# Optimization experiments

Hardware: AMD Instinct MI355X
Metric: run time of the kernel (lower is better)

## Reference

```python
import jax, jax.numpy as jnp
import numpy as np

N_HASHES = 4
CHUNK = 144
REDUCTION = 4
RES_SCALE = 1.0
NORM_EPS = 5e-5


def conv2d(x, w, b, pad):
    y = jax.lax.conv_general_dilated(
        x, w, window_strides=(1, 1), padding=[(pad, pad), (pad, pad)],
        dimension_numbers=('NCHW', 'OIHW', 'NCHW'))
    return y + b[None, :, None, None]


def add_adjacent_buckets(x):
    # x: (N, h, n_chunks, chunk, e); concat each chunk with its circular neighbors
    back = jnp.roll(x, 1, axis=2)
    fwd = jnp.roll(x, -1, axis=2)
    return jnp.concatenate([x, back, fwd], axis=3)


def setup_inputs() -> dict:
    key = jax.random.key(0)
    ks = jax.random.split(key, 6)
    x = jax.random.normal(ks[0], (1, 32, 192, 192), jnp.float32)
    w_match = jax.random.normal(ks[1], (8, 32, 3, 3), jnp.float32) * 0.05
    b_match = jnp.zeros((8,), jnp.float32)
    w_asm = jax.random.normal(ks[2], (32, 32, 1, 1), jnp.float32) * 0.05
    b_asm = jnp.zeros((32,), jnp.float32)
    rotations = jax.random.normal(ks[3], (8, N_HASHES, 64), jnp.float32)
    return {'x': x, 'w_match': w_match, 'b_match': b_match,
            'w_asm': w_asm, 'b_asm': b_asm, 'rotations': rotations}


def reference(x, w_match, b_match, w_asm, b_asm, rotations):
    N, _, H, W = x.shape
    L = H * W
    # conv_match: 3x3 conv 32->8; conv_assembly: 1x1 conv 32->32
    x_embed = conv2d(x, w_match, b_match, 1).reshape(N, -1, L).transpose(0, 2, 1)  # (N, L, 8)
    y_embed = conv2d(x, w_asm, b_asm, 0).reshape(N, -1, L).transpose(0, 2, 1)      # (N, L, 32)
    C = x_embed.shape[-1]
    hash_buckets = min(L // CHUNK + (L // CHUNK) % 2, 128)  # = 128 here

    # --- LSH hashing (non-differentiable; rotations passed in for determinism) ---
    rotated = jnp.einsum('blf,fhi->bhli', x_embed, rotations)        # (N, h, L, hb/2)
    rotated = jnp.concatenate([rotated, -rotated], axis=-1)          # (N, h, L, hb)
    hash_codes = jnp.argmax(rotated, axis=-1)                        # (N, h, L)
    hash_codes = hash_codes + (jnp.arange(N_HASHES) * hash_buckets)[None, :, None]
    hash_codes = hash_codes.reshape(N, -1)                           # (N, h*L)

    # --- sort tokens by bucket id ---
    indices = jnp.argsort(hash_codes, axis=-1)
    undo_sort = jnp.argsort(indices, axis=-1)
    mod_indices = indices % L
    x_sorted = jnp.take_along_axis(x_embed, mod_indices[:, :, None], axis=1)  # (N, h*L, 8)
    y_sorted = jnp.take_along_axis(y_embed, mod_indices[:, :, None], axis=1)  # (N, h*L, 32)

    x_b = x_sorted.reshape(N, N_HASHES, -1, C)
    y_b = y_sorted.reshape(N, N_HASHES, -1, C * REDUCTION)
    padding = (-L) % CHUNK  # static; 0 for L=192*192
    if padding:
        x_b = jnp.concatenate([x_b, x_b[:, :, -padding:, :]], axis=2)
        y_b = jnp.concatenate([y_b, y_b[:, :, -padding:, :]], axis=2)
    x_b = x_b.reshape(N, N_HASHES, -1, CHUNK, C)
    y_b = y_b.reshape(N, N_HASHES, -1, CHUNK, C * REDUCTION)

    # --- bucketed attention with adjacent buckets ---
    nrm = jnp.linalg.norm(x_b, axis=-1, keepdims=True)
    x_match = x_b / jnp.maximum(nrm, NORM_EPS)   # F.normalize(eps=5e-5)
    x_match = add_adjacent_buckets(x_match)      # (N, h, k, 3*chunk, 8)
    y_adj = add_adjacent_buckets(y_b)            # (N, h, k, 3*chunk, 32)

    raw = jnp.einsum('bhkie,bhkje->bhkij', x_b, x_match)  # (N, h, k, 144, 432)
    bucket_score = jax.scipy.special.logsumexp(raw, axis=-1, keepdims=True)
    score = jnp.exp(raw - bucket_score)
    ret = jnp.einsum('bhkij,bhkje->bhkie', score, y_adj)  # (N, h, k, 144, 32)

    ret = ret.reshape(N, N_HASHES, -1, C * REDUCTION)
    bucket_score = bucket_score.reshape(N, N_HASHES, -1)
    if padding:
        ret = ret[:, :, :-padding, :]
        bucket_score = bucket_score[:, :, :-padding]
    ret = ret.reshape(N, -1, C * REDUCTION)
    bucket_score = bucket_score.reshape(N, -1)

    # --- unsort and combine hash rounds via softmax over logsumexp scores ---
    ret = jnp.take_along_axis(ret, undo_sort[:, :, None], axis=1)
    bucket_score = jnp.take_along_axis(bucket_score, undo_sort, axis=1)
    ret = ret.reshape(N, N_HASHES, L, C * REDUCTION)
    probs = jax.nn.softmax(bucket_score.reshape(N, N_HASHES, L, 1), axis=1)
    out = jnp.sum(ret * probs, axis=1)                     # (N, L, 32)
    out = out.transpose(0, 2, 1).reshape(N, -1, H, W) * RES_SCALE + x
    return out
```

## Files before the change

### kernel.cpp

```cpp
#include <hip/hip_runtime.h>
#include <hip/hip_bf16.h>
#include <math.h>

#define LTOT 36864
#define NH 4
#define NCHUNK 256
#define CHU 144
#define NBUCK 128
#define NSEG 144
#define HW_ 192
#define VTS 148

typedef unsigned int u32;
typedef unsigned short u16;
typedef unsigned long long u64;
typedef __attribute__((ext_vector_type(4))) short short4v;
typedef __attribute__((ext_vector_type(4))) float f32x4;

__device__ __forceinline__ u32 pkbf(float a, float b){
  union { __hip_bfloat162 h2; u32 u; } cv;
  cv.h2 = __float22bfloat162_rn(float2{a,b});
  return cv.u;
}
__device__ __forceinline__ float bflo(u32 w){ return __uint_as_float(w<<16); }
__device__ __forceinline__ float bfhi(u32 w){ return __uint_as_float(w & 0xffff0000u); }

__global__ __launch_bounds__(256) void k_conv(const float* __restrict__ x,
    const float* __restrict__ wm, const float* __restrict__ bm,
    const float* __restrict__ wa, const float* __restrict__ ba,
    float* __restrict__ xe, float* __restrict__ ye)
{
  __shared__ float xs[32*108];
  const int t = threadIdx.x;
  const int id = blockIdx.x;

  if (id < 576){
    const int bx = id % 12, by = id / 12;
    for (int idx=t; idx<3456; idx+=256){
      int ci = idx/108, rem = idx-ci*108;
      int iy = rem/18,  ix = rem-iy*18;
      int yy = by*4+iy-1, xx = bx*16+ix-1;
      float v = 0.f;
      if (yy>=0 && yy<HW_ && xx>=0 && xx<HW_) v = x[ci*LTOT + yy*HW_ + xx];
      xs[idx] = v;
    }
    __syncthreads();
    const int lane = t & 63;
    const int co0 = __builtin_amdgcn_readfirstlane((t>>6)<<1);
    const int ix = lane & 15, iy = lane >> 4;
    float a0 = bm[co0], a1 = bm[co0+1];
    const float* xb  = xs + iy*18 + ix;
    const float* w0p = wm + co0*288;
    const float* w1p = w0p + 288;
    for (int ci=0; ci<32; ci++){
      const float* xp = xb + ci*108;
      float x00=xp[0],  x01=xp[1],  x02=xp[2];
      float x10=xp[18], x11=xp[19], x12=xp[20];
      float x20=xp[36], x21=xp[37], x22=xp[38];
      const float* w0 = w0p + ci*9;
      const float* w1 = w1p + ci*9;
      a0 += x00*w0[0]+x01*w0[1]+x02*w0[2]
          + x10*w0[3]+x11*w0[4]+x12*w0[5]
          + x20*w0[6]+x21*w0[7]+x22*w0[8];
      a1 += x00*w1[0]+x01*w1[1]+x02*w1[2]
          + x10*w1[3]+x11*w1[4]+x12*w1[5]
          + x20*w1[6]+x21*w1[7]+x22*w1[8];
    }
    const int l = (by*4+iy)*HW_ + bx*16+ix;
    *(float2*)(xe + l*8 + co0) = float2{a0,a1};
  } else {
    const int zid = id - 576;
    const int cb = (zid/144)*8;
    const int l  = (zid%144)*256 + t;
    float acc[8];
    #pragma unroll
    for (int co=0;co<8;co++) acc[co] = ba[cb+co];
    #pragma unroll 4
    for (int ci=0; ci<32; ci++){
      float xv = x[ci*LTOT + l];
      #pragma unroll
      for (int co=0;co<8;co++) acc[co] += xv * wa[(cb+co)*32 + ci];
    }
    float4* yp = (float4*)(ye + l*32 + cb);
    yp[0] = make_float4(acc[0],acc[1],acc[2],acc[3]);
    yp[1] = make_float4(acc[4],acc[5],acc[6],acc[7]);
  }
}

__global__ __launch_bounds__(256) void k_hashrank(const float* __restrict__ xe,
    const float* __restrict__ rot, int* __restrict__ code,
    int* __restrict__ lrank, int* __restrict__ hist)
{
  const int h = blockIdx.y, seg = blockIdx.x, t = threadIdx.x;
  const int l = seg*256 + t;
  const float4* qp = (const float4*)(xe + l*8);
  float4 qa = qp[0], qb = qp[1];
  float best = -INFINITY; int bi = 0;
  float worst = INFINITY; int wi = 0;
  for (int i=0; i<64; i++){
    const float* rp = rot + h*64 + i;
    float v = qa.x*rp[0]    + qa.y*rp[256]  + qa.z*rp[512]  + qa.w*rp[768]
            + qb.x*rp[1024] + qb.y*rp[1280] + qb.z*rp[1536] + qb.w*rp[1792];
    if (v > best)  { best  = v; bi = i; }
    if (v < worst) { worst = v; wi = i; }
  }
  int c = (-worst > best) ? (64+wi) : bi;
  code[h*LTOT + l] = c;

  const int lane = t & 63, w = t >> 6;
  u64 mask = ~0ull;
  #pragma unroll
  for (int bit=0; bit<7; bit++){
    u64 bset = __ballot((c>>bit)&1);
    mask &= ((c>>bit)&1) ? bset : ~bset;
  }
  int rin = __popcll(mask & ((lane==0)?0ull:(~0ull >> (64-lane))));
  int cnt = __popcll(mask);

  __shared__ int wh[4][NBUCK];
  ((int*)wh)[t] = 0; ((int*)wh)[t+256] = 0;
  __syncthreads();
  if (rin == 0) wh[w][c] = cnt;
  __syncthreads();
  int r = rin;
  for (int ww=0; ww<w; ww++) r += wh[ww][c];
  lrank[h*LTOT + l] = r;
  if (t < NBUCK) hist[(h*NSEG+seg)*NBUCK + t] = wh[0][t]+wh[1][t]+wh[2][t]+wh[3][t];
}

__global__ __launch_bounds__(512) void k_scan(const int* __restrict__ hist,
    int* __restrict__ segoff)
{
  const int h = blockIdx.x;
  const int b = threadIdx.x & 127, g = threadIdx.x >> 7;
  int vals[36];
  int sum = 0;
  #pragma unroll
  for (int i=0;i<36;i++){
    vals[i] = hist[(h*NSEG + g*36 + i)*NBUCK + b];
    sum += vals[i];
  }
  __shared__ int ps[4][NBUCK];
  __shared__ int tot[NBUCK];
  __shared__ int scv[NBUCK];
  ps[g][b] = sum;
  __syncthreads();
  if (g == 0){
    int run = 0;
    #pragma unroll
    for (int gg=0; gg<4; gg++){ int tv = ps[gg][b]; ps[gg][b] = run; run += tv; }
    tot[b] = run;
    int v = run;
    #pragma unroll
    for (int off=1; off<64; off<<=1){
      int u = __shfl_up(v, off);
      if ((b & 63) >= off) v += u;
    }
    scv[b] = v;
  }
  __syncthreads();
  int base = scv[b] - tot[b] + ((b >= 64) ? scv[63] : 0);
  int run2 = base + ps[g][b];
  #pragma unroll
  for (int i=0;i<36;i++){
    segoff[(h*NSEG + g*36 + i)*NBUCK + b] = run2;
    run2 += vals[i];
  }
}

__global__ __launch_bounds__(256) void k_scatter(const int* __restrict__ code,
    const int* __restrict__ lrank, const int* __restrict__ segoff,
    const float* __restrict__ xe, const float* __restrict__ ye,
    int* __restrict__ rankof, u16* __restrict__ Ks, u16* __restrict__ Qs,
    u16* __restrict__ Vs)
{
  const int h = blockIdx.y, seg = blockIdx.x, t = threadIdx.x;
  const int l = seg*256 + t;
  int c = code[h*LTOT + l];
  int r = segoff[(h*NSEG+seg)*NBUCK + c] + lrank[h*LTOT + l];
  rankof[h*LTOT + l] = r;

  const float4* xr = (const float4*)(xe + l*8);
  float4 a = xr[0], b = xr[1];
  float n2 = a.x*a.x+a.y*a.y+a.z*a.z+a.w*a.w
           + b.x*b.x+b.y*b.y+b.z*b.z+b.w*b.w;
  float sc = 1.0f / fmaxf(sqrtf(n2), 5e-5f);
  uint4 kk, qq;
  kk.x = pkbf(a.x*sc,a.y*sc); kk.y = pkbf(a.z*sc,a.w*sc);
  kk.z = pkbf(b.x*sc,b.y*sc); kk.w = pkbf(b.z*sc,b.w*sc);
  qq.x = pkbf(a.x,a.y); qq.y = pkbf(a.z,a.w);
  qq.z = pkbf(b.x,b.y); qq.w = pkbf(b.z,b.w);
  *(uint4*)(Ks + (size_t)(h*LTOT + r)*8) = kk;
  *(uint4*)(Qs + (size_t)(h*LTOT + r)*8) = qq;

  const float4* yr = (const float4*)(ye + l*32);
  uint4* vp = (uint4*)(Vs + (size_t)(h*LTOT + r)*32);
  #pragma unroll
  for (int e4=0; e4<4; e4++){
    float4 v0 = yr[2*e4], v1 = yr[2*e4+1];
    uint4 w;
    w.x = pkbf(v0.x,v0.y); w.y = pkbf(v0.z,v0.w);
    w.z = pkbf(v1.x,v1.y); w.w = pkbf(v1.z,v1.w);
    vp[e4] = w;
  }
}

__global__ __launch_bounds__(320) void k_attn(const u16* __restrict__ Ks,
    const u16* __restrict__ Qs, const u16* __restrict__ Vs,
    u16* __restrict__ ret_s, float* __restrict__ bs_s)
{
  __shared__ __align__(16) u16 Klds[CHU*8];
  __shared__ __align__(16) u16 Qlds[CHU*8];
  __shared__ __align__(16) u16 VT[32*VTS];
  __shared__ float qn[CHU];

  const int t = threadIdx.x;
  const int k = blockIdx.x, h = blockIdx.y;

  if (t < CHU){
    uint4 qv = *(const uint4*)(Qs + (size_t)(h*LTOT + k*CHU + t)*8);
    *(uint4*)(Qlds + t*8) = qv;
    float f0=bflo(qv.x), f1=bfhi(qv.x), f2=bflo(qv.y), f3=bfhi(qv.y);
    float f4=bflo(qv.z), f5=bfhi(qv.z), f6=bflo(qv.w), f7=bfhi(qv.w);
    float n2 = f0*f0+f1*f1+f2*f2+f3*f3+f4*f4+f5*f5+f6*f6+f7*f7;
    qn[t] = sqrtf(n2)*1.01f + 1e-6f;
  }
  __syncthreads();

  const int lane = t & 63;
  const int wv = t >> 6;
  const int q = lane & 15;
  const int quad = lane >> 4;
  const int tl0 = 2*wv, tl1 = (2*wv+1 < 9) ? 2*wv+1 : 8;

  const short4v zs = {0,0,0,0};
  short4v bq0 = zs, bq1 = zs;
  if (quad < 2){
    bq0 = *(const short4v*)(Qlds + (tl0*16+q)*8 + quad*4);
    bq1 = *(const short4v*)(Qlds + (tl1*16+q)*8 + quad*4);
  }
  const float m0 = qn[tl0*16+q], m1 = qn[tl1*16+q];

  f32x4 o00={0,0,0,0}, o01={0,0,0,0}, o10={0,0,0,0}, o11={0,0,0,0};
  float s0 = 0.f, s1 = 0.f;

  for (int r=0; r<3; r++){
    __syncthreads();
    const int gkb = ((k + NCHUNK-1 + r) & (NCHUNK-1)) * CHU;
    if (t < CHU){
      *(uint4*)(Klds + t*8) = *(const uint4*)(Ks + (size_t)(h*LTOT + gkb + t)*8);
    } else if (t >= 176){
      int i = t - 176;
      int p = i >> 1, hf = i & 1;
      const uint4* ra = (const uint4*)(Vs + (size_t)(h*LTOT + gkb + 2*p)*32);
      const uint4* rb = (const uint4*)(Vs + (size_t)(h*LTOT + gkb + 2*p+1)*32);
      uint4 A0 = ra[hf*2], A1 = ra[hf*2+1];
      uint4 B0 = rb[hf*2], B1 = rb[hf*2+1];
      u32 aw[8] = {A0.x,A0.y,A0.z,A0.w,A1.x,A1.y,A1.z,A1.w};
      u32 bw[8] = {B0.x,B0.y,B0.z,B0.w,B1.x,B1.y,B1.z,B1.w};
      int ebase = hf*16;
      #pragma unroll
      for (int m=0;m<8;m++){
        u32 al = aw[m]&0xffffu, ah = aw[m]>>16;
        u32 bl = bw[m]&0xffffu, bh = bw[m]>>16;
        *(u32*)&VT[(ebase+2*m  )*VTS + 2*p] = al | (bl<<16);
        *(u32*)&VT[(ebase+2*m+1)*VTS + 2*p] = ah | (bh<<16);
      }
    }
    __syncthreads();

    #pragma unroll 3
    for (int kt=0; kt<9; kt++){
      short4v av = zs;
      if (quad < 2) av = *(const short4v*)(Klds + (kt*16+q)*8 + quad*4);
      f32x4 zc = {0.f,0.f,0.f,0.f};
      f32x4 stA = __builtin_amdgcn_mfma_f32_16x16x16bf16_1k(av, bq0, zc, 0,0,0);
      f32x4 stB = __builtin_amdgcn_mfma_f32_16x16x16bf16_1k(av, bq1, zc, 0,0,0);

      float pA0 = __expf(stA[0]-m0), pA1 = __expf(stA[1]-m0);
      float pA2 = __expf(stA[2]-m0), pA3 = __expf(stA[3]-m0);
      float pB0 = __expf(stB[0]-m1), pB1 = __expf(stB[1]-m1);
      float pB2 = __expf(stB[2]-m1), pB3 = __expf(stB[3]-m1);
      s0 += (pA0+pA1)+(pA2+pA3);
      s1 += (pB0+pB1)+(pB2+pB3);

      union { u32 u[2]; short4v s4; } pkA, pkB;
      pkA.u[0] = pkbf(pA0,pA1); pkA.u[1] = pkbf(pA2,pA3);
      pkB.u[0] = pkbf(pB0,pB1); pkB.u[1] = pkbf(pB2,pB3);

      short4v va0 = *(const short4v*)(&VT[ q    *VTS + kt*16 + quad*4]);
      short4v va1 = *(const short4v*)(&VT[(q+16)*VTS + kt*16 + quad*4]);
      o00 = __builtin_amdgcn_mfma_f32_16x16x16bf16_1k(va0, pkA.s4, o00, 0,0,0);
      o01 = __builtin_amdgcn_mfma_f32_16x16x16bf16_1k(va1, pkA.s4, o01, 0,0,0);
      o10 = __builtin_amdgcn_mfma_f32_16x16x16bf16_1k(va0, pkB.s4, o10, 0,0,0);
      o11 = __builtin_amdgcn_mfma_f32_16x16x16bf16_1k(va1, pkB.s4, o11, 0,0,0);
    }
  }

  float st0 = s0, st1 = s1;
  st0 += __shfl_xor(st0, 16); st0 += __shfl_xor(st0, 32);
  st1 += __shfl_xor(st1, 16); st1 += __shfl_xor(st1, 32);
  float inv0 = 1.0f/st0, inv1 = 1.0f/st1;

  const int row0 = h*LTOT + k*CHU + tl0*16 + q;
  const int row1 = h*LTOT + k*CHU + tl1*16 + q;
  u16* rp0 = ret_s + (size_t)row0*32;
  u16* rp1 = ret_s + (size_t)row1*32;
  uint2 wA, wB;
  wA.x = pkbf(o00[0]*inv0, o00[1]*inv0); wA.y = pkbf(o00[2]*inv0, o00[3]*inv0);
  wB.x = pkbf(o01[0]*inv0, o01[1]*inv0); wB.y = pkbf(o01[2]*inv0, o01[3]*inv0);
  *(uint2*)&rp0[quad*4]    = wA;
  *(uint2*)&rp0[16+quad*4] = wB;
  wA.x = pkbf(o10[0]*inv1, o10[1]*inv1); wA.y = pkbf(o10[2]*inv1, o10[3]*inv1);
  wB.x = pkbf(o11[0]*inv1, o11[1]*inv1); wB.y = pkbf(o11[2]*inv1, o11[3]*inv1);
  *(uint2*)&rp1[quad*4]    = wA;
  *(uint2*)&rp1[16+quad*4] = wB;
  if (quad == 0){
    bs_s[row0] = m0 + __logf(st0);
    bs_s[row1] = m1 + __logf(st1);
  }
}

__global__ __launch_bounds__(256) void k_final(const float* __restrict__ x,
    const int* __restrict__ rankof, const u16* __restrict__ ret_s,
    const float* __restrict__ bs_s, float* __restrict__ out)
{
  const int l  = blockIdx.x*64 + (threadIdx.x & 63);
  const int eg = threadIdx.x >> 6;
  int r[NH]; float bs[NH];
  #pragma unroll
  for (int h=0;h<NH;h++) r[h] = rankof[h*LTOT + l];
  #pragma unroll
  for (int h=0;h<NH;h++) bs[h] = bs_s[h*LTOT + r[h]];
  float m = fmaxf(fmaxf(bs[0],bs[1]), fmaxf(bs[2],bs[3]));
  float p[NH]; float s = 0.f;
  #pragma unroll
  for (int h=0;h<NH;h++){ p[h] = __expf(bs[h]-m); s += p[h]; }
  float inv = 1.0f/s;
  float o[8];
  #pragma unroll
  for (int e=0;e<8;e++) o[e]=0.f;
  #pragma unroll
  for (int h=0;h<NH;h++){
    float w = p[h]*inv;
    uint4 v = *(const uint4*)(ret_s + (size_t)(h*LTOT + r[h])*32 + eg*8);
    o[0] += w*bflo(v.x); o[1] += w*bfhi(v.x);
    o[2] += w*bflo(v.y); o[3] += w*bfhi(v.y);
    o[4] += w*bflo(v.z); o[5] += w*bfhi(v.z);
    o[6] += w*bflo(v.w); o[7] += w*bfhi(v.w);
  }
  #pragma unroll
  for (int e=0;e<8;e++){
    int ge = eg*8 + e;
    out[ge*LTOT + l] = o[e] + x[ge*LTOT + l];
  }
}

extern "C" void kernel_launch(void* const* d_in, const int* in_sizes, int n_in,
                              void* d_out, int out_size, void* d_ws, size_t ws_size,
                              hipStream_t stream)
{
  const float* x   = (const float*)d_in[0];
  const float* wm  = (const float*)d_in[1];
  const float* bm  = (const float*)d_in[2];
  const float* wa  = (const float*)d_in[3];
  const float* ba  = (const float*)d_in[4];
  const float* rot = (const float*)d_in[5];
  float* out = (float*)d_out;

  char* ws = (char*)d_ws;
  size_t off = 0;
  auto alloc = [&](size_t bytes)->void*{
    void* p = ws + off;
    off = (off + bytes + 255) & ~(size_t)255;
    return p;
  };
  float* xe     = (float*)alloc((size_t)LTOT*8*4);
  float* ye     = (float*)alloc((size_t)LTOT*32*4);
  int*   code   = (int*)  alloc((size_t)NH*LTOT*4);
  int*   lrank  = (int*)  alloc((size_t)NH*LTOT*4);
  int*   hist   = (int*)  alloc((size_t)NH*NSEG*NBUCK*4);
  int*   segoff = (int*)  alloc((size_t)NH*NSEG*NBUCK*4);
  int*   rankof = (int*)  alloc((size_t)NH*LTOT*4);
  u16*   Ks     = (u16*)  alloc((size_t)NH*LTOT*8*2);
  u16*   Qs     = (u16*)  alloc((size_t)NH*LTOT*8*2);
  u16*   Vs     = (u16*)  alloc((size_t)NH*LTOT*32*2);
  u16*   ret_s  = (u16*)  alloc((size_t)NH*LTOT*32*2);
  float* bs_s   = (float*)alloc((size_t)NH*LTOT*4);

  hipLaunchKernelGGL(k_conv,     dim3(1152),       dim3(256), 0, stream, x, wm, bm, wa, ba, xe, ye);
  hipLaunchKernelGGL(k_hashrank, dim3(NSEG,NH),    dim3(256), 0, stream, xe, rot, code, lrank, hist);
  hipLaunchKernelGGL(k_scan,     dim3(NH),         dim3(512), 0, stream, hist, segoff);
  hipLaunchKernelGGL(k_scatter,  dim3(NSEG,NH),    dim3(256), 0, stream, code, lrank, segoff, xe, ye, rankof, Ks, Qs, Vs);
  hipLaunchKernelGGL(k_attn,     dim3(NCHUNK,NH),  dim3(320), 0, stream, Ks, Qs, Vs, ret_s, bs_s);
  hipLaunchKernelGGL(k_final,    dim3(576),        dim3(256), 0, stream, x, rankof, ret_s, bs_s, out);
}
```

Measured before the change: 137.5 us.

## Fuse 1x1 conv into 3x3 conv tiles and prefetch next K/V chunk in attention

The 1x1 assembly conv is merged into the 3x3 conv blocks, reusing the center pixel already staged in shared memory, so the separate blocks that reread x from global memory are gone and the grid is halved. In the attention kernel, the K/V chunk for the next neighbor round is loaded into registers before the MFMA loop over the current chunk and written to LDS afterwards. This hides global load latency behind compute. The costs are extra registers for the prefetched data and fewer conv blocks, each doing more work.

```diff
diff --git a/kernel.cpp b/kernel.cpp
--- a/kernel.cpp
+++ b/kernel.cpp
@@ -33,58 +33,51 @@
   __shared__ float xs[32*108];
   const int t = threadIdx.x;
   const int id = blockIdx.x;
-
-  if (id < 576){
-    const int bx = id % 12, by = id / 12;
-    for (int idx=t; idx<3456; idx+=256){
-      int ci = idx/108, rem = idx-ci*108;
-      int iy = rem/18,  ix = rem-iy*18;
-      int yy = by*4+iy-1, xx = bx*16+ix-1;
-      float v = 0.f;
-      if (yy>=0 && yy<HW_ && xx>=0 && xx<HW_) v = x[ci*LTOT + yy*HW_ + xx];
-      xs[idx] = v;
-    }
-    __syncthreads();
-    const int lane = t & 63;
-    const int co0 = __builtin_amdgcn_readfirstlane((t>>6)<<1);
-    const int ix = lane & 15, iy = lane >> 4;
-    float a0 = bm[co0], a1 = bm[co0+1];
-    const float* xb  = xs + iy*18 + ix;
-    const float* w0p = wm + co0*288;
-    const float* w1p = w0p + 288;
-    for (int ci=0; ci<32; ci++){
-      const float* xp = xb + ci*108;
-      float x00=xp[0],  x01=xp[1],  x02=xp[2];
-      float x10=xp[18], x11=xp[19], x12=xp[20];
-      float x20=xp[36], x21=xp[37], x22=xp[38];
-      const float* w0 = w0p + ci*9;
-      const float* w1 = w1p + ci*9;
-      a0 += x00*w0[0]+x01*w0[1]+x02*w0[2]
-          + x10*w0[3]+x11*w0[4]+x12*w0[5]
-          + x20*w0[6]+x21*w0[7]+x22*w0[8];
-      a1 += x00*w1[0]+x01*w1[1]+x02*w1[2]
-          + x10*w1[3]+x11*w1[4]+x12*w1[5]
-          + x20*w1[6]+x21*w1[7]+x22*w1[8];
-    }
-    const int l = (by*4+iy)*HW_ + bx*16+ix;
-    *(float2*)(xe + l*8 + co0) = float2{a0,a1};
-  } else {
-    const int zid = id - 576;
-    const int cb = (zid/144)*8;
-    const int l  = (zid%144)*256 + t;
-    float acc[8];
+  const int bx = id % 12, by = id / 12;
+
+  for (int idx=t; idx<3456; idx+=256){
+    int ci = idx/108, rem = idx-ci*108;
+    int iy = rem/18,  ix = rem-iy*18;
+    int yy = by*4+iy-1, xx = bx*16+ix-1;
+    float v = 0.f;
+    if (yy>=0 && yy<HW_ && xx>=0 && xx<HW_) v = x[ci*LTOT + yy*HW_ + xx];
+    xs[idx] = v;
+  }
+  __syncthreads();
+  const int lane = t & 63;
+  const int w  = __builtin_amdgcn_readfirstlane(t>>6);
+  const int co0 = 2*w;
+  const int cb  = 8*w;
+  const int ix = lane & 15, iy = lane >> 4;
+  float a0 = bm[co0], a1 = bm[co0+1];
+  float acc[8];
+  #pragma unroll
+  for (int co=0;co<8;co++) acc[co] = ba[cb+co];
+  const float* xb  = xs + iy*18 + ix;
+  const float* w0p = wm + co0*288;
+  const float* w1p = w0p + 288;
+  for (int ci=0; ci<32; ci++){
+    const float* xp = xb + ci*108;
+    float x00=xp[0],  x01=xp[1],  x02=xp[2];
+    float x10=xp[18], x11=xp[19], x12=xp[20];
+    float x20=xp[36], x21=xp[37], x22=xp[38];
+    const float* w0 = w0p + ci*9;
+    const float* w1 = w1p + ci*9;
+    a0 += x00*w0[0]+x01*w0[1]+x02*w0[2]
+        + x10*w0[3]+x11*w0[4]+x12*w0[5]
+        + x20*w0[6]+x21*w0[7]+x22*w0[8];
+    a1 += x00*w1[0]+x01*w1[1]+x02*w1[2]
+        + x10*w1[3]+x11*w1[4]+x12*w1[5]
+        + x20*w1[6]+x21*w1[7]+x22*w1[8];
+    const float* wap = wa + cb*32 + ci;
     #pragma unroll
-    for (int co=0;co<8;co++) acc[co] = ba[cb+co];
-    #pragma unroll 4
-    for (int ci=0; ci<32; ci++){
-      float xv = x[ci*LTOT + l];
-      #pragma unroll
-      for (int co=0;co<8;co++) acc[co] += xv * wa[(cb+co)*32 + ci];
-    }
-    float4* yp = (float4*)(ye + l*32 + cb);
-    yp[0] = make_float4(acc[0],acc[1],acc[2],acc[3]);
-    yp[1] = make_float4(acc[4],acc[5],acc[6],acc[7]);
-  }
+    for (int co=0;co<8;co++) acc[co] += x11 * wap[co*32];
+  }
+  const int l = (by*4+iy)*HW_ + bx*16+ix;
+  *(float2*)(xe + l*8 + co0) = float2{a0,a1};
+  float4* yp = (float4*)(ye + l*32 + cb);
+  yp[0] = make_float4(acc[0],acc[1],acc[2],acc[3]);
+  yp[1] = make_float4(acc[4],acc[5],acc[6],acc[7]);
 }
 
 __global__ __launch_bounds__(256) void k_hashrank(const float* __restrict__ xe,
@@ -217,13 +210,39 @@
   const int t = threadIdx.x;
   const int k = blockIdx.x, h = blockIdx.y;
 
+  uint4 kpref;
+  uint4 vpa0, vpa1, vpb0, vpb1;
+  const int vp_i = t - 176, vp_p = vp_i >> 1, vp_hf = vp_i & 1;
+
+  {
+    const int gkb = ((k + NCHUNK-1) & (NCHUNK-1)) * CHU;
+    if (t < CHU){
+      kpref = *(const uint4*)(Ks + (size_t)(h*LTOT + gkb + t)*8);
+      uint4 qv = *(const uint4*)(Qs + (size_t)(h*LTOT + k*CHU + t)*8);
+      *(uint4*)(Qlds + t*8) = qv;
+      float f0=bflo(qv.x), f1=bfhi(qv.x), f2=bflo(qv.y), f3=bfhi(qv.y);
+      float f4=bflo(qv.z), f5=bfhi(qv.z), f6=bflo(qv.w), f7=bfhi(qv.w);
+      qn[t] = sqrtf(f0*f0+f1*f1+f2*f2+f3*f3+f4*f4+f5*f5+f6*f6+f7*f7)*1.01f + 1e-6f;
+    } else if (t >= 176){
+      const uint4* ra = (const uint4*)(Vs + (size_t)(h*LTOT + gkb + 2*vp_p)*32);
+      const uint4* rb = (const uint4*)(Vs + (size_t)(h*LTOT + gkb + 2*vp_p+1)*32);
+      vpa0 = ra[vp_hf*2]; vpa1 = ra[vp_hf*2+1];
+      vpb0 = rb[vp_hf*2]; vpb1 = rb[vp_hf*2+1];
+    }
+  }
   if (t < CHU){
-    uint4 qv = *(const uint4*)(Qs + (size_t)(h*LTOT + k*CHU + t)*8);
-    *(uint4*)(Qlds + t*8) = qv;
-    float f0=bflo(qv.x), f1=bfhi(qv.x), f2=bflo(qv.y), f3=bfhi(qv.y);
-    float f4=bflo(qv.z), f5=bfhi(qv.z), f6=bflo(qv.w), f7=bfhi(qv.w);
-    float n2 = f0*f0+f1*f1+f2*f2+f3*f3+f4*f4+f5*f5+f6*f6+f7*f7;
-    qn[t] = sqrtf(n2)*1.01f + 1e-6f;
+    *(uint4*)(Klds + t*8) = kpref;
+  } else if (t >= 176){
+    u32 aw[8] = {vpa0.x,vpa0.y,vpa0.z,vpa0.w,vpa1.x,vpa1.y,vpa1.z,vpa1.w};
+    u32 bw[8] = {vpb0.x,vpb0.y,vpb0.z,vpb0.w,vpb1.x,vpb1.y,vpb1.z,vpb1.w};
+    int ebase = vp_hf*16;
+    #pragma unroll
+    for (int m=0;m<8;m++){
+      u32 al = aw[m]&0xffffu, ah = aw[m]>>16;
+      u32 bl = bw[m]&0xffffu, bh = bw[m]>>16;
+      *(u32*)&VT[(ebase+2*m  )*VTS + 2*vp_p] = al | (bl<<16);
+      *(u32*)&VT[(ebase+2*m+1)*VTS + 2*vp_p] = ah | (bh<<16);
+    }
   }
   __syncthreads();
 
@@ -245,29 +264,17 @@
   float s0 = 0.f, s1 = 0.f;
 
   for (int r=0; r<3; r++){
-    __syncthreads();
-    const int gkb = ((k + NCHUNK-1 + r) & (NCHUNK-1)) * CHU;
-    if (t < CHU){
-      *(uint4*)(Klds + t*8) = *(const uint4*)(Ks + (size_t)(h*LTOT + gkb + t)*8);
-    } else if (t >= 176){
-      int i = t - 176;
-      int p = i >> 1, hf = i & 1;
-      const uint4* ra = (const uint4*)(Vs + (size_t)(h*LTOT + gkb + 2*p)*32);
-      const uint4* rb = (const uint4*)(Vs + (size_t)(h*LTOT + gkb + 2*p+1)*32);
-      uint4 A0 = ra[hf*2], A1 = ra[hf*2+1];
-      uint4 B0 = rb[hf*2], B1 = rb[hf*2+1];
-      u32 aw[8] = {A0.x,A0.y,A0.z,A0.w,A1.x,A1.y,A1.z,A1.w};
-      u32 bw[8] = {B0.x,B0.y,B0.z,B0.w,B1.x,B1.y,B1.z,B1.w};
-      int ebase = hf*16;
-      #pragma unroll
-      for (int m=0;m<8;m++){
-        u32 al = aw[m]&0xffffu, ah = aw[m]>>16;
-        u32 bl = bw[m]&0xffffu, bh = bw[m]>>16;
-        *(u32*)&VT[(ebase+2*m  )*VTS + 2*p] = al | (bl<<16);
-        *(u32*)&VT[(ebase+2*m+1)*VTS + 2*p] = ah | (bh<<16);
+    if (r < 2){
+      const int gkb = ((k + NCHUNK + r) & (NCHUNK-1)) * CHU;
+      if (t < CHU){
+        kpref = *(const uint4*)(Ks + (size_t)(h*LTOT + gkb + t)*8);
+      } else if (t >= 176){
+        const uint4* ra = (const uint4*)(Vs + (size_t)(h*LTOT + gkb + 2*vp_p)*32);
+        const uint4* rb = (const uint4*)(Vs + (size_t)(h*LTOT + gkb + 2*vp_p+1)*32);
+        vpa0 = ra[vp_hf*2]; vpa1 = ra[vp_hf*2+1];
+        vpb0 = rb[vp_hf*2]; vpb1 = rb[vp_hf*2+1];
       }
     }
-    __syncthreads();
 
     #pragma unroll 3
     for (int kt=0; kt<9; kt++){
@@ -294,6 +301,25 @@
       o01 = __builtin_amdgcn_mfma_f32_16x16x16bf16_1k(va1, pkA.s4, o01, 0,0,0);
       o10 = __builtin_amdgcn_mfma_f32_16x16x16bf16_1k(va0, pkB.s4, o10, 0,0,0);
       o11 = __builtin_amdgcn_mfma_f32_16x16x16bf16_1k(va1, pkB.s4, o11, 0,0,0);
+    }
+
+    if (r < 2){
+      __syncthreads();
+      if (t < CHU){
+        *(uint4*)(Klds + t*8) = kpref;
+      } else if (t >= 176){
+        u32 aw[8] = {vpa0.x,vpa0.y,vpa0.z,vpa0.w,vpa1.x,vpa1.y,vpa1.z,vpa1.w};
+        u32 bw[8] = {vpb0.x,vpb0.y,vpb0.z,vpb0.w,vpb1.x,vpb1.y,vpb1.z,vpb1.w};
+        int ebase = vp_hf*16;
+        #pragma unroll
+        for (int m=0;m<8;m++){
+          u32 al = aw[m]&0xffffu, ah = aw[m]>>16;
+          u32 bl = bw[m]&0xffffu, bh = bw[m]>>16;
+          *(u32*)&VT[(ebase+2*m  )*VTS + 2*vp_p] = al | (bl<<16);
+          *(u32*)&VT[(ebase+2*m+1)*VTS + 2*vp_p] = ah | (bh<<16);
+        }
+      }
+      __syncthreads();
     }
   }
 
@@ -388,7 +414,7 @@
   u16*   ret_s  = (u16*)  alloc((size_t)NH*LTOT*32*2);
   float* bs_s   = (float*)alloc((size_t)NH*LTOT*4);
 
-  hipLaunchKernelGGL(k_conv,     dim3(1152),       dim3(256), 0, stream, x, wm, bm, wa, ba, xe, ye);
+  hipLaunchKernelGGL(k_conv,     dim3(576),        dim3(256), 0, stream, x, wm, bm, wa, ba, xe, ye);
   hipLaunchKernelGGL(k_hashrank, dim3(NSEG,NH),    dim3(256), 0, stream, xe, rot, code, lrank, hist);
   hipLaunchKernelGGL(k_scan,     dim3(NH),         dim3(512), 0, stream, hist, segoff);
   hipLaunchKernelGGL(k_scatter,  dim3(NSEG,NH),    dim3(256), 0, stream, code, lrank, segoff, xe, ye, rankof, Ks, Qs, Vs);
```

After: 140.2 us. Within noise of the previous version (+1.9%).

## Fuse 1x1 conv into 3x3 conv, scatter attention outputs to unsorted positions

Applied to the files above, without the earlier changes.

The 1x1 assembly conv is now computed inside the 3x3 conv blocks, reusing the shared-memory center pixel and writing bf16 values directly. The scatter kernel then copies them instead of converting. The attention kernel writes its outputs and logsumexp scores straight to original token positions through an inverse permutation, so the final kernel reads contiguously with no rank gather. The last wave also skips the duplicated ninth tile. The trade-offs are scattered writes in attention and heavier per-thread work in the conv kernel.

```diff
diff --git a/kernel.cpp b/kernel.cpp
--- a/kernel.cpp
+++ b/kernel.cpp
@@ -28,63 +28,56 @@
 __global__ __launch_bounds__(256) void k_conv(const float* __restrict__ x,
     const float* __restrict__ wm, const float* __restrict__ bm,
     const float* __restrict__ wa, const float* __restrict__ ba,
-    float* __restrict__ xe, float* __restrict__ ye)
+    float* __restrict__ xe, u16* __restrict__ Vu)
 {
   __shared__ float xs[32*108];
   const int t = threadIdx.x;
   const int id = blockIdx.x;
-
-  if (id < 576){
-    const int bx = id % 12, by = id / 12;
-    for (int idx=t; idx<3456; idx+=256){
-      int ci = idx/108, rem = idx-ci*108;
-      int iy = rem/18,  ix = rem-iy*18;
-      int yy = by*4+iy-1, xx = bx*16+ix-1;
-      float v = 0.f;
-      if (yy>=0 && yy<HW_ && xx>=0 && xx<HW_) v = x[ci*LTOT + yy*HW_ + xx];
-      xs[idx] = v;
-    }
-    __syncthreads();
-    const int lane = t & 63;
-    const int co0 = __builtin_amdgcn_readfirstlane((t>>6)<<1);
-    const int ix = lane & 15, iy = lane >> 4;
-    float a0 = bm[co0], a1 = bm[co0+1];
-    const float* xb  = xs + iy*18 + ix;
-    const float* w0p = wm + co0*288;
-    const float* w1p = w0p + 288;
-    for (int ci=0; ci<32; ci++){
-      const float* xp = xb + ci*108;
-      float x00=xp[0],  x01=xp[1],  x02=xp[2];
-      float x10=xp[18], x11=xp[19], x12=xp[20];
-      float x20=xp[36], x21=xp[37], x22=xp[38];
-      const float* w0 = w0p + ci*9;
-      const float* w1 = w1p + ci*9;
-      a0 += x00*w0[0]+x01*w0[1]+x02*w0[2]
-          + x10*w0[3]+x11*w0[4]+x12*w0[5]
-          + x20*w0[6]+x21*w0[7]+x22*w0[8];
-      a1 += x00*w1[0]+x01*w1[1]+x02*w1[2]
-          + x10*w1[3]+x11*w1[4]+x12*w1[5]
-          + x20*w1[6]+x21*w1[7]+x22*w1[8];
-    }
-    const int l = (by*4+iy)*HW_ + bx*16+ix;
-    *(float2*)(xe + l*8 + co0) = float2{a0,a1};
-  } else {
-    const int zid = id - 576;
-    const int cb = (zid/144)*8;
-    const int l  = (zid%144)*256 + t;
-    float acc[8];
+  const int bx = id % 12, by = id / 12;
+
+  for (int idx=t; idx<3456; idx+=256){
+    int ci = idx/108, rem = idx-ci*108;
+    int iy = rem/18,  ix = rem-iy*18;
+    int yy = by*4+iy-1, xx = bx*16+ix-1;
+    float v = 0.f;
+    if (yy>=0 && yy<HW_ && xx>=0 && xx<HW_) v = x[ci*LTOT + yy*HW_ + xx];
+    xs[idx] = v;
+  }
+  __syncthreads();
+  const int lane = t & 63;
+  const int w  = __builtin_amdgcn_readfirstlane(t>>6);
+  const int co0 = 2*w, cb = 8*w;
+  const int ix = lane & 15, iy = lane >> 4;
+  float a0 = bm[co0], a1 = bm[co0+1];
+  float acc[8];
+  #pragma unroll
+  for (int co=0;co<8;co++) acc[co] = ba[cb+co];
+  const float* xb  = xs + iy*18 + ix;
+  const float* w0p = wm + co0*288;
+  const float* w1p = w0p + 288;
+  for (int ci=0; ci<32; ci++){
+    const float* xp = xb + ci*108;
+    float x00=xp[0],  x01=xp[1],  x02=xp[2];
+    float x10=xp[18], x11=xp[19], x12=xp[20];
+    float x20=xp[36], x21=xp[37], x22=xp[38];
+    const float* w0 = w0p + ci*9;
+    const float* w1 = w1p + ci*9;
+    a0 += x00*w0[0]+x01*w0[1]+x02*w0[2]
+        + x10*w0[3]+x11*w0[4]+x12*w0[5]
+        + x20*w0[6]+x21*w0[7]+x22*w0[8];
+    a1 += x00*w1[0]+x01*w1[1]+x02*w1[2]
+        + x10*w1[3]+x11*w1[4]+x12*w1[5]
+        + x20*w1[6]+x21*w1[7]+x22*w1[8];
+    const float* wap = wa + cb*32 + ci;
     #pragma unroll
-    for (int co=0;co<8;co++) acc[co] = ba[cb+co];
-    #pragma unroll 4
-    for (int ci=0; ci<32; ci++){
-      float xv = x[ci*LTOT + l];
-      #pragma unroll
-      for (int co=0;co<8;co++) acc[co] += xv * wa[(cb+co)*32 + ci];
-    }
-    float4* yp = (float4*)(ye + l*32 + cb);
-    yp[0] = make_float4(acc[0],acc[1],acc[2],acc[3]);
-    yp[1] = make_float4(acc[4],acc[5],acc[6],acc[7]);
-  }
+    for (int co=0;co<8;co++) acc[co] += x11 * wap[co*32];
+  }
+  const int l = (by*4+iy)*HW_ + bx*16+ix;
+  *(float2*)(xe + l*8 + co0) = float2{a0,a1};
+  uint4 vv;
+  vv.x = pkbf(acc[0],acc[1]); vv.y = pkbf(acc[2],acc[3]);
+  vv.z = pkbf(acc[4],acc[5]); vv.w = pkbf(acc[6],acc[7]);
+  *(uint4*)(Vu + (size_t)l*32 + cb) = vv;
 }
 
 __global__ __launch_bounds__(256) void k_hashrank(const float* __restrict__ xe,
@@ -170,15 +163,15 @@
 
 __global__ __launch_bounds__(256) void k_scatter(const int* __restrict__ code,
     const int* __restrict__ lrank, const int* __restrict__ segoff,
-    const float* __restrict__ xe, const float* __restrict__ ye,
-    int* __restrict__ rankof, u16* __restrict__ Ks, u16* __restrict__ Qs,
+    const float* __restrict__ xe, const u16* __restrict__ Vu,
+    int* __restrict__ spos, u16* __restrict__ Ks, u16* __restrict__ Qs,
     u16* __restrict__ Vs)
 {
   const int h = blockIdx.y, seg = blockIdx.x, t = threadIdx.x;
   const int l = seg*256 + t;
   int c = code[h*LTOT + l];
   int r = segoff[(h*NSEG+seg)*NBUCK + c] + lrank[h*LTOT + l];
-  rankof[h*LTOT + l] = r;
+  spos[h*LTOT + r] = l;
 
   const float4* xr = (const float4*)(xe + l*8);
   float4 a = xr[0], b = xr[1];
@@ -193,26 +186,20 @@
   *(uint4*)(Ks + (size_t)(h*LTOT + r)*8) = kk;
   *(uint4*)(Qs + (size_t)(h*LTOT + r)*8) = qq;
 
-  const float4* yr = (const float4*)(ye + l*32);
+  const uint4* vr = (const uint4*)(Vu + (size_t)l*32);
   uint4* vp = (uint4*)(Vs + (size_t)(h*LTOT + r)*32);
-  #pragma unroll
-  for (int e4=0; e4<4; e4++){
-    float4 v0 = yr[2*e4], v1 = yr[2*e4+1];
-    uint4 w;
-    w.x = pkbf(v0.x,v0.y); w.y = pkbf(v0.z,v0.w);
-    w.z = pkbf(v1.x,v1.y); w.w = pkbf(v1.z,v1.w);
-    vp[e4] = w;
-  }
+  vp[0] = vr[0]; vp[1] = vr[1]; vp[2] = vr[2]; vp[3] = vr[3];
 }
 
 __global__ __launch_bounds__(320) void k_attn(const u16* __restrict__ Ks,
     const u16* __restrict__ Qs, const u16* __restrict__ Vs,
-    u16* __restrict__ ret_s, float* __restrict__ bs_s)
+    const int* __restrict__ spos, u16* __restrict__ ret_u, float* __restrict__ bs_u)
 {
   __shared__ __align__(16) u16 Klds[CHU*8];
   __shared__ __align__(16) u16 Qlds[CHU*8];
   __shared__ __align__(16) u16 VT[32*VTS];
   __shared__ float qn[CHU];
+  __shared__ int spos_l[CHU];
 
   const int t = threadIdx.x;
   const int k = blockIdx.x, h = blockIdx.y;
@@ -222,8 +209,8 @@
     *(uint4*)(Qlds + t*8) = qv;
     float f0=bflo(qv.x), f1=bfhi(qv.x), f2=bflo(qv.y), f3=bfhi(qv.y);
     float f4=bflo(qv.z), f5=bfhi(qv.z), f6=bflo(qv.w), f7=bfhi(qv.w);
-    float n2 = f0*f0+f1*f1+f2*f2+f3*f3+f4*f4+f5*f5+f6*f6+f7*f7;
-    qn[t] = sqrtf(n2)*1.01f + 1e-6f;
+    qn[t] = sqrtf(f0*f0+f1*f1+f2*f2+f3*f3+f4*f4+f5*f5+f6*f6+f7*f7)*1.01f + 1e-6f;
+    spos_l[t] = spos[h*LTOT + k*CHU + t];
   }
   __syncthreads();
 
@@ -231,15 +218,18 @@
   const int wv = t >> 6;
   const int q = lane & 15;
   const int quad = lane >> 4;
-  const int tl0 = 2*wv, tl1 = (2*wv+1 < 9) ? 2*wv+1 : 8;
+  const bool two = (wv < 4);
+  const int tl0 = 2*wv;
+  const int tl1 = two ? (2*wv+1) : 8;
 
   const short4v zs = {0,0,0,0};
   short4v bq0 = zs, bq1 = zs;
   if (quad < 2){
     bq0 = *(const short4v*)(Qlds + (tl0*16+q)*8 + quad*4);
-    bq1 = *(const short4v*)(Qlds + (tl1*16+q)*8 + quad*4);
-  }
-  const float m0 = qn[tl0*16+q], m1 = qn[tl1*16+q];
+    if (two) bq1 = *(const short4v*)(Qlds + (tl1*16+q)*8 + quad*4);
+  }
+  const float m0 = qn[tl0*16+q];
+  const float m1 = two ? qn[tl1*16+q] : 0.f;
 
   f32x4 o00={0,0,0,0}, o01={0,0,0,0}, o10={0,0,0,0}, o11={0,0,0,0};
   float s0 = 0.f, s1 = 0.f;
@@ -275,63 +265,67 @@
       if (quad < 2) av = *(const short4v*)(Klds + (kt*16+q)*8 + quad*4);
       f32x4 zc = {0.f,0.f,0.f,0.f};
       f32x4 stA = __builtin_amdgcn_mfma_f32_16x16x16bf16_1k(av, bq0, zc, 0,0,0);
-      f32x4 stB = __builtin_amdgcn_mfma_f32_16x16x16bf16_1k(av, bq1, zc, 0,0,0);
 
       float pA0 = __expf(stA[0]-m0), pA1 = __expf(stA[1]-m0);
       float pA2 = __expf(stA[2]-m0), pA3 = __expf(stA[3]-m0);
-      float pB0 = __expf(stB[0]-m1), pB1 = __expf(stB[1]-m1);
-      float pB2 = __expf(stB[2]-m1), pB3 = __expf(stB[3]-m1);
       s0 += (pA0+pA1)+(pA2+pA3);
-      s1 += (pB0+pB1)+(pB2+pB3);
-
-      union { u32 u[2]; short4v s4; } pkA, pkB;
+      union { u32 u[2]; short4v s4; } pkA;
       pkA.u[0] = pkbf(pA0,pA1); pkA.u[1] = pkbf(pA2,pA3);
-      pkB.u[0] = pkbf(pB0,pB1); pkB.u[1] = pkbf(pB2,pB3);
 
       short4v va0 = *(const short4v*)(&VT[ q    *VTS + kt*16 + quad*4]);
       short4v va1 = *(const short4v*)(&VT[(q+16)*VTS + kt*16 + quad*4]);
       o00 = __builtin_amdgcn_mfma_f32_16x16x16bf16_1k(va0, pkA.s4, o00, 0,0,0);
       o01 = __builtin_amdgcn_mfma_f32_16x16x16bf16_1k(va1, pkA.s4, o01, 0,0,0);
-      o10 = __builtin_amdgcn_mfma_f32_16x16x16bf16_1k(va0, pkB.s4, o10, 0,0,0);
-      o11 = __builtin_amdgcn_mfma_f32_16x16x16bf16_1k(va1, pkB.s4, o11, 0,0,0);
+
+      if (two){
+        f32x4 stB = __builtin_amdgcn_mfma_f32_16x16x16bf16_1k(av, bq1, zc, 0,0,0);
+        float pB0 = __expf(stB[0]-m1), pB1 = __expf(stB[1]-m1);
+        float pB2 = __expf(stB[2]-m1), pB3 = __expf(stB[3]-m1);
+        s1 += (pB0+pB1)+(pB2+pB3);
+        union { u32 u[2]; short4v s4; } pkB;
+        pkB.u[0] = pkbf(pB0,pB1); pkB.u[1] = pkbf(pB2,pB3);
+        o10 = __builtin_amdgcn_mfma_f32_16x16x16bf16_1k(va0, pkB.s4, o10, 0,0,0);
+        o11 = __builtin_amdgcn_mfma_f32_16x16x16bf16_1k(va1, pkB.s4, o11, 0,0,0);
+      }
     }
   }
 
-  float st0 = s0, st1 = s1;
+  float st0 = s0;
   st0 += __shfl_xor(st0, 16); st0 += __shfl_xor(st0, 32);
-  st1 += __shfl_xor(st1, 16); st1 += __shfl_xor(st1, 32);
-  float inv0 = 1.0f/st0, inv1 = 1.0f/st1;
-
-  const int row0 = h*LTOT + k*CHU + tl0*16 + q;
-  const int row1 = h*LTOT + k*CHU + tl1*16 + q;
-  u16* rp0 = ret_s + (size_t)row0*32;
-  u16* rp1 = ret_s + (size_t)row1*32;
+  float inv0 = 1.0f/st0;
+
+  const int pos0 = spos_l[tl0*16 + q];
+  u16* rp0 = ret_u + (size_t)(h*LTOT + pos0)*32;
   uint2 wA, wB;
   wA.x = pkbf(o00[0]*inv0, o00[1]*inv0); wA.y = pkbf(o00[2]*inv0, o00[3]*inv0);
   wB.x = pkbf(o01[0]*inv0, o01[1]*inv0); wB.y = pkbf(o01[2]*inv0, o01[3]*inv0);
   *(uint2*)&rp0[quad*4]    = wA;
   *(uint2*)&rp0[16+quad*4] = wB;
-  wA.x = pkbf(o10[0]*inv1, o10[1]*inv1); wA.y = pkbf(o10[2]*inv1, o10[3]*inv1);
-  wB.x = pkbf(o11[0]*inv1, o11[1]*inv1); wB.y = pkbf(o11[2]*inv1, o11[3]*inv1);
-  *(uint2*)&rp1[quad*4]    = wA;
-  *(uint2*)&rp1[16+quad*4] = wB;
-  if (quad == 0){
-    bs_s[row0] = m0 + __logf(st0);
-    bs_s[row1] = m1 + __logf(st1);
+  if (quad == 0) bs_u[h*LTOT + pos0] = m0 + __logf(st0);
+
+  if (two){
+    float st1 = s1;
+    st1 += __shfl_xor(st1, 16); st1 += __shfl_xor(st1, 32);
+    float inv1 = 1.0f/st1;
+    const int pos1 = spos_l[tl1*16 + q];
+    u16* rp1 = ret_u + (size_t)(h*LTOT + pos1)*32;
+    wA.x = pkbf(o10[0]*inv1, o10[1]*inv1); wA.y = pkbf(o10[2]*inv1, o10[3]*inv1);
+    wB.x = pkbf(o11[0]*inv1, o11[1]*inv1); wB.y = pkbf(o11[2]*inv1, o11[3]*inv1);
+    *(uint2*)&rp1[quad*4]    = wA;
+    *(uint2*)&rp1[16+quad*4] = wB;
+    if (quad == 0) bs_u[h*LTOT + pos1] = m1 + __logf(st1);
   }
 }
 
 __global__ __launch_bounds__(256) void k_final(const float* __restrict__ x,
-    const int* __restrict__ rankof, const u16* __restrict__ ret_s,
-    const float* __restrict__ bs_s, float* __restrict__ out)
+    const u16* __restrict__ ret_u, const float* __restrict__ bs_u,
+    float* __restrict__ out)
 {
   const int l  = blockIdx.x*64 + (threadIdx.x & 63);
   const int eg = threadIdx.x >> 6;
-  int r[NH]; float bs[NH];
-  #pragma unroll
-  for (int h=0;h<NH;h++) r[h] = rankof[h*LTOT + l];
-  #pragma unroll
-  for (int h=0;h<NH;h++) bs[h] = bs_s[h*LTOT + r[h]];
+  float bs[NH];
+  #pragma unroll
+  for (int h=0;h<NH;h++) bs[h] = bs_u[h*LTOT + l];
   float m = fmaxf(fmaxf(bs[0],bs[1]), fmaxf(bs[2],bs[3]));
   float p[NH]; float s = 0.f;
   #pragma unroll
@@ -343,7 +337,7 @@
   #pragma unroll
   for (int h=0;h<NH;h++){
     float w = p[h]*inv;
-    uint4 v = *(const uint4*)(ret_s + (size_t)(h*LTOT + r[h])*32 + eg*8);
+    uint4 v = *(const uint4*)(ret_u + (size_t)(h*LTOT + l)*32 + eg*8);
     o[0] += w*bflo(v.x); o[1] += w*bfhi(v.x);
     o[2] += w*bflo(v.y); o[3] += w*bfhi(v.y);
     o[4] += w*bflo(v.z); o[5] += w*bfhi(v.z);
@@ -376,22 +370,22 @@
     return p;
   };
   float* xe     = (float*)alloc((size_t)LTOT*8*4);
-  float* ye     = (float*)alloc((size_t)LTOT*32*4);
+  u16*   Vu     = (u16*)  alloc((size_t)LTOT*32*2);
   int*   code   = (int*)  alloc((size_t)NH*LTOT*4);
   int*   lrank  = (int*)  alloc((size_t)NH*LTOT*4);
   int*   hist   = (int*)  alloc((size_t)NH*NSEG*NBUCK*4);
   int*   segoff = (int*)  alloc((size_t)NH*NSEG*NBUCK*4);
-  int*   rankof = (int*)  alloc((size_t)NH*LTOT*4);
+  int*   spos   = (int*)  alloc((size_t)NH*LTOT*4);
   u16*   Ks     = (u16*)  alloc((size_t)NH*LTOT*8*2);
   u16*   Qs     = (u16*)  alloc((size_t)NH*LTOT*8*2);
   u16*   Vs     = (u16*)  alloc((size_t)NH*LTOT*32*2);
-  u16*   ret_s  = (u16*)  alloc((size_t)NH*LTOT*32*2);
-  float* bs_s   = (float*)alloc((size_t)NH*LTOT*4);
-
-  hipLaunchKernelGGL(k_conv,     dim3(1152),       dim3(256), 0, stream, x, wm, bm, wa, ba, xe, ye);
+  u16*   ret_u  = (u16*)  alloc((size_t)NH*LTOT*32*2);
+  float* bs_u   = (float*)alloc((size_t)NH*LTOT*4);
+
+  hipLaunchKernelGGL(k_conv,     dim3(576),        dim3(256), 0, stream, x, wm, bm, wa, ba, xe, Vu);
   hipLaunchKernelGGL(k_hashrank, dim3(NSEG,NH),    dim3(256), 0, stream, xe, rot, code, lrank, hist);
   hipLaunchKernelGGL(k_scan,     dim3(NH),         dim3(512), 0, stream, hist, segoff);
-  hipLaunchKernelGGL(k_scatter,  dim3(NSEG,NH),    dim3(256), 0, stream, code, lrank, segoff, xe, ye, rankof, Ks, Qs, Vs);
-  hipLaunchKernelGGL(k_attn,     dim3(NCHUNK,NH),  dim3(320), 0, stream, Ks, Qs, Vs, ret_s, bs_s);
-  hipLaunchKernelGGL(k_final,    dim3(576),        dim3(256), 0, stream, x, rankof, ret_s, bs_s, out);
-}
+  hipLaunchKernelGGL(k_scatter,  dim3(NSEG,NH),    dim3(256), 0, stream, code, lrank, segoff, xe, Vu, spos, Ks, Qs, Vs);
+  hipLaunchKernelGGL(k_attn,     dim3(NCHUNK,NH),  dim3(320), 0, stream, Ks, Qs, Vs, spos, ret_u, bs_u);
+  hipLaunchKernelGGL(k_final,    dim3(576),        dim3(256), 0, stream, x, ret_u, bs_u, out);
+}
```

Result: faster. 130.5 us (-5.1%).
